# Optimization experiments

Measured on AMD Instinct MI355X. Metric: run time of the kernel, lower is better.

## Reference

```python
import jax, jax.numpy as jnp
import numpy as np

# S5 layer: ZOH discretization of diagonal complex SSM + parallel associative scan
# u: (B, L, H) real; state dim P (complex diagonal Lambda)

DT_MIN, DT_MAX = 1e-3, 1e-1
STEP_RESCALE = 1.0

def setup_inputs() -> dict:
    key = jax.random.key(0)
    ks = jax.random.split(key, 7)
    Bsz, L, H, P = 8, 4096, 1024, 512
    u = jax.random.normal(ks[0], (Bsz, L, H), jnp.float32)
    # HiPPO-like diagonal: negative real part, spread imaginary part
    Lambda_re = -0.5 * jnp.abs(jax.random.normal(ks[1], (P,), jnp.float32)) - 0.1
    Lambda_im = jnp.pi * jax.random.normal(ks[2], (P,), jnp.float32)
    # B: (P, H, 2) real/imag stacked (xavier-ish scale); C: (H, P, 2)
    Bp = jax.random.normal(ks[3], (P, H, 2), jnp.float32) / np.sqrt(H)
    Cp = jax.random.normal(ks[4], (H, P, 2), jnp.float32) / np.sqrt(P)
    D = jax.random.normal(ks[5], (H,), jnp.float32)
    log_step = jnp.log(jax.random.uniform(ks[6], (P, 1), jnp.float32) * (DT_MAX - DT_MIN) + DT_MIN)
    return {"u": u, "Lambda_re": Lambda_re, "Lambda_im": Lambda_im,
            "B": Bp, "C": Cp, "D": D, "log_step": log_step}


def _s5_forward(u, Lambda_re, Lambda_im, B, C, D, log_step):
    # clip_eigs=True: keep real part strictly negative
    Lambda = jnp.minimum(Lambda_re, -1e-4) + 1j * Lambda_im          # (P,)
    B_tilde = (B[..., 0] + 1j * B[..., 1]).astype(jnp.complex64)      # (P, H)
    C_tilde = (C[..., 0] + 1j * C[..., 1]).astype(jnp.complex64)      # (H, P)
    step = STEP_RESCALE * jnp.exp(log_step[:, 0])                     # (P,)
    # ZOH discretization
    Lambda_bar = jnp.exp(Lambda * step)                               # (P,)
    B_bar = ((Lambda_bar - 1.0) / Lambda)[:, None] * B_tilde          # (P, H)
    # input projection into state space
    Bu = jnp.einsum('blh,ph->blp', u.astype(jnp.complex64), B_bar)    # (B, L, P)
    A = jnp.broadcast_to(Lambda_bar, Bu.shape)                        # (B, L, P)
    # linear recurrence x_k = Lambda_bar * x_{k-1} + Bu_k via log-depth scan
    def combine(e_i, e_j):
        a_i, b_i = e_i
        a_j, b_j = e_j
        return a_j * a_i, a_j * b_i + b_j
    _, xs = jax.lax.associative_scan(combine, (A, Bu), axis=1)        # (B, L, P)
    # readout
    ys = jnp.einsum('blp,hp->blh', xs, C_tilde).real + D * u          # (B, L, H)
    return ys


def reference(u, Lambda_re, Lambda_im, B, C, D, log_step):
    return _s5_forward(u, Lambda_re, Lambda_im, B, C, D, log_step)
```

## Files before the change

kernel.cpp:

```cpp
#include <hip/hip_runtime.h>


#define Bsz 8
#define Lseq 4096
#define Hdim 1024
#define Pdim 512
#define NCHUNK 64
#define CHUNK 64
#define MROWS 32768

typedef __attribute__((ext_vector_type(8))) __bf16 bf16x8;
typedef __attribute__((ext_vector_type(4))) float f32x4;

__device__ __forceinline__ unsigned short f2bf(float f) {
  union { float f; unsigned u; } v; v.f = f;
  unsigned r = v.u + 0x7fffu + ((v.u >> 16) & 1u);
  return (unsigned short)(r >> 16);
}
__device__ __forceinline__ float bf2f(unsigned short s) {
  union { unsigned u; float f; } v; v.u = ((unsigned)s) << 16;
  return v.f;
}

__device__ __forceinline__ void gld_lds16(const void* g, void* l) {
  __builtin_amdgcn_global_load_lds(
      (const __attribute__((address_space(1))) unsigned int*)g,
      (__attribute__((address_space(3))) unsigned int*)l, 16, 0, 0);
}

__global__ void k_setup(const float* __restrict__ Lre_in, const float* __restrict__ Lim_in,
                        const float* __restrict__ log_step,
                        float2* __restrict__ a_arr, float2* __restrict__ aS_arr,
                        float2* __restrict__ g_arr) {
  int p = threadIdx.x;
  if (p >= Pdim) return;
  float lre = fminf(Lre_in[p], -1e-4f);
  float lim = Lim_in[p];
  float step = expf(log_step[p]);
  float zr = lre * step, zi = lim * step;
  float er = expf(zr);
  float ar = er * cosf(zi), ai = er * sinf(zi);
  a_arr[p] = make_float2(ar, ai);
  float erS = expf(zr * (float)CHUNK);
  aS_arr[p] = make_float2(erS * cosf(zi * (float)CHUNK), erS * sinf(zi * (float)CHUNK));
  float den = lre * lre + lim * lim;
  float nr = ar - 1.0f, ni = ai;
  g_arr[p] = make_float2((nr * lre + ni * lim) / den, (ni * lre - nr * lim) / den);
}

__global__ void k_prep_B(const float* __restrict__ Bin, const float2* __restrict__ g_arr,
                         unsigned short* __restrict__ Bbar2) {
  int idx = blockIdx.x * 256 + threadIdx.x;
  int p = idx >> 10;
  int h = idx & 1023;
  float B0 = Bin[2 * idx];
  float B1 = Bin[2 * idx + 1];
  float2 g = g_arr[p];
  Bbar2[(size_t)p * Hdim + h]            = f2bf(g.x * B0 - g.y * B1);
  Bbar2[(size_t)(Pdim + p) * Hdim + h]   = f2bf(g.x * B1 + g.y * B0);
}

__global__ void k_prep_C(const float* __restrict__ Cin, unsigned short* __restrict__ C2m) {
  int idx = blockIdx.x * 256 + threadIdx.x;
  int h = idx >> 9;
  int p = idx & 511;
  float C0 = Cin[2 * idx];
  float C1 = Cin[2 * idx + 1];
  C2m[(size_t)h * 1024 + p]        = f2bf(C0);
  C2m[(size_t)h * 1024 + 512 + p]  = f2bf(-C1);
}

__global__ void k_cvt_u(const float* __restrict__ u, unsigned short* __restrict__ ub) {
  size_t tidg = (size_t)blockIdx.x * 256 + threadIdx.x;
#pragma unroll 4
  for (int it = 0; it < 16; ++it) {
    size_t i = (tidg + (size_t)it * 524288) * 4;
    float4 v = *(const float4*)(u + i);
    ushort4 o;
    o.x = f2bf(v.x); o.y = f2bf(v.y); o.z = f2bf(v.z); o.w = f2bf(v.w);
    *(ushort4*)(ub + i) = o;
  }
}


#define STAGE_A(t_, bo_)                                                    \
  do {                                                                      \
    _Pragma("unroll")                                                       \
    for (int jj = 0; jj < 4; jj++)                                          \
      gld_lds16(pa[jj] + (t_) * 64, smc + (bo_) + (jj * 512 + tid) * 16);   \
  } while (0)

#define STAGE_B(t_, bo_)                                                    \
  do {                                                                      \
    _Pragma("unroll")                                                       \
    for (int jj = 0; jj < 4; jj++)                                          \
      gld_lds16(pb[jj] + (t_) * 64, smc + (bo_) + 32768 + (jj * 512 + tid) * 16); \
  } while (0)

#define PHASE_Q(mh, nh, LA, LB, PRE, POST)                                  \
  {                                                                         \
    const char* bb_ = smc + bufo;                                           \
    if (LA) {                                                               \
      _Pragma("unroll")                                                     \
      for (int i_ = 0; i_ < 4; i_++) {                                      \
        int rb_ = aRowByte + ((mh) * 4 + i_) * 2048;                        \
        af[i_][0] = *(const bf16x8*)(bb_ + rb_ + k0);                       \
        af[i_][1] = *(const bf16x8*)(bb_ + rb_ + k1);                       \
      }                                                                     \
    }                                                                       \
    if (LB) {                                                               \
      _Pragma("unroll")                                                     \
      for (int j_ = 0; j_ < 2; j_++) {                                      \
        int rb_ = bRowByte + ((nh) * 2 + j_) * 2048;                        \
        bfv[j_][0] = *(const bf16x8*)(bb_ + rb_ + k0);                      \
        bfv[j_][1] = *(const bf16x8*)(bb_ + rb_ + k1);                      \
      }                                                                     \
    }                                                                       \
    PRE;                                                                    \
    __builtin_amdgcn_s_barrier();                                           \
    asm volatile("s_waitcnt lgkmcnt(0)" ::: "memory");                      \
    __builtin_amdgcn_sched_barrier(0);                                      \
    __builtin_amdgcn_s_setprio(1);                                          \
    _Pragma("unroll")                                                       \
    for (int i_ = 0; i_ < 4; i_++)                                          \
      _Pragma("unroll")                                                     \
      for (int j_ = 0; j_ < 2; j_++) {                                      \
        acc[(mh) * 4 + i_][(nh) * 2 + j_] =                                 \
            __builtin_amdgcn_mfma_f32_16x16x32_bf16(                        \
                af[i_][0], bfv[j_][0], acc[(mh) * 4 + i_][(nh) * 2 + j_], 0, 0, 0); \
        acc[(mh) * 4 + i_][(nh) * 2 + j_] =                                 \
            __builtin_amdgcn_mfma_f32_16x16x32_bf16(                        \
                af[i_][1], bfv[j_][1], acc[(mh) * 4 + i_][(nh) * 2 + j_], 0, 0, 0); \
      }                                                                     \
    __builtin_amdgcn_s_setprio(0);                                          \
    POST;                                                                   \
    __builtin_amdgcn_s_barrier();                                           \
  }

template <int EPI>
__global__ __launch_bounds__(512, 2) void gemm256(const unsigned short* __restrict__ A,
                                                  const unsigned short* __restrict__ Bt,
                                                  void* __restrict__ Cout,
                                                  const float* __restrict__ uin,
                                                  const float* __restrict__ Dvec) {
  const int K = 1024;
  __shared__ __align__(16) unsigned short sm[65536];
  char* smc = (char*)sm;

  int tid = threadIdx.x;
  int lane = tid & 63;
  int w = tid >> 6;
  int wr = w >> 2, wc = w & 3;
  int quad = lane >> 4;
  int mrow = lane & 15;

  int wg = blockIdx.x;
  size_t rowBase = (size_t)(wg >> 2) * 256;
  size_t colBase = (size_t)(wg & 3) * 256;

  f32x4 acc[8][4];
#pragma unroll
  for (int i = 0; i < 8; i++)
#pragma unroll
    for (int j = 0; j < 4; j++) acc[i][j] = (f32x4){0.f, 0.f, 0.f, 0.f};

  bf16x8 af[4][2], bfv[2][2];

  int cs = (tid & 7) ^ ((tid >> 3) & 7);
  int rT = tid >> 3;
  const unsigned short* pa[4];
  const unsigned short* pb[4];
#pragma unroll
  for (int jj = 0; jj < 4; jj++) {
    pa[jj] = A  + (rowBase + jj * 64 + rT) * K + cs * 8;
    pb[jj] = Bt + (colBase + jj * 64 + rT) * K + cs * 8;
  }

  int axor = (mrow & 7) << 4;
  int k0 = (quad * 16) ^ axor;
  int k1 = (64 + quad * 16) ^ axor;
  int aRowByte = (wr * 128 + mrow) * 128;
  int bRowByte = 32768 + (wc * 64 + mrow) * 128;

  STAGE_A(0, 0);
  STAGE_B(0, 0);
  asm volatile("s_waitcnt vmcnt(0)" ::: "memory");
  __builtin_amdgcn_s_barrier();

  for (int t = 0; t < 16; ++t) {
    int bufo = (t & 1) * 65536;
    int nbo = bufo ^ 65536;
    PHASE_Q(0, 0, 1, 1, if (t < 15) STAGE_A(t + 1, nbo), );
    PHASE_Q(0, 1, 0, 1, if (t < 15) STAGE_B(t + 1, nbo), );
    PHASE_Q(1, 1, 1, 0, , );
    PHASE_Q(1, 0, 0, 1, , asm volatile("s_waitcnt vmcnt(0)" ::: "memory"));
  }

  if (EPI == 0) {
    unsigned short* O = (unsigned short*)Cout;
    __syncthreads();
#pragma unroll
    for (int fm = 0; fm < 8; fm++)
#pragma unroll
      for (int fn = 0; fn < 4; fn++)
#pragma unroll
        for (int r = 0; r < 4; r++) {
          int m_l = wr * 128 + fm * 16 + quad * 4 + r;
          int n_l = wc * 64 + fn * 16 + mrow;
          sm[m_l * 256 + n_l] = f2bf(acc[fm][fn][r]);
        }
    __syncthreads();
#pragma unroll
    for (int it = 0; it < 16; it++) {
      int cid = it * 512 + tid;
      int r = cid >> 5;
      int c = cid & 31;
      uint4 v = *(const uint4*)(sm + r * 256 + c * 8);
      *(uint4*)(O + (rowBase + r) * 1024 + colBase + c * 8) = v;
    }
  } else {
    float* O = (float*)Cout;
    size_t mBase = rowBase + wr * 128 + quad * 4;
    size_t nBase = colBase + wc * 64 + mrow;
#pragma unroll
    for (int fm = 0; fm < 8; fm++)
#pragma unroll
      for (int fn = 0; fn < 4; fn++) {
        size_t n = nBase + fn * 16;
        float dv = Dvec[n];
#pragma unroll
        for (int r = 0; r < 4; r++) {
          size_t m = mBase + fm * 16 + r;
          O[m * 1024 + n] = acc[fm][fn][r] + dv * uin[m * 1024 + n];
        }
      }
  }
}

__global__ void k_scan1(const unsigned short* __restrict__ Bu, const float2* __restrict__ a_arr,
                        float* __restrict__ carryT) {
  int bc = blockIdx.x;
  int p0 = threadIdx.x * 2;
  int b = bc >> 6, c = bc & 63;
  float2 a0 = a_arr[p0], a1 = a_arr[p0 + 1];
  const unsigned short* bu = Bu + ((size_t)b * Lseq + (size_t)c * CHUNK) * 1024;
  float tr0 = 0.f, ti0 = 0.f, tr1 = 0.f, ti1 = 0.f;
#pragma unroll 8
  for (int l = 0; l < CHUNK; l++) {
    unsigned vr = *(const unsigned*)(bu + (size_t)l * 1024 + p0);
    unsigned vi = *(const unsigned*)(bu + (size_t)l * 1024 + 512 + p0);
    float br0 = bf2f((unsigned short)vr), br1 = bf2f((unsigned short)(vr >> 16));
    float bi0 = bf2f((unsigned short)vi), bi1 = bf2f((unsigned short)(vi >> 16));
    float nr0 = fmaf(a0.x, tr0, fmaf(-a0.y, ti0, br0));
    ti0 = fmaf(a0.x, ti0, fmaf(a0.y, tr0, bi0));
    tr0 = nr0;
    float nr1 = fmaf(a1.x, tr1, fmaf(-a1.y, ti1, br1));
    ti1 = fmaf(a1.x, ti1, fmaf(a1.y, tr1, bi1));
    tr1 = nr1;
  }
  *(float2*)(carryT + (size_t)bc * 1024 + p0) = make_float2(tr0, tr1);
  *(float2*)(carryT + (size_t)bc * 1024 + 512 + p0) = make_float2(ti0, ti1);
}

__global__ void k_scan2(const float* __restrict__ carryT, const float2* __restrict__ aS_arr,
                        float* __restrict__ prefix) {
  int wid = blockIdx.x * 4 + (threadIdx.x >> 6);
  int lane = threadIdx.x & 63;
  int b = wid >> 9;
  int p = wid & 511;
  float2 s = aS_arr[p];
  size_t o = ((size_t)(b * NCHUNK + lane)) * 1024 + p;
  float tr = carryT[o], ti = carryT[o + 512];
  float mr = s.x, mi = s.y;
#pragma unroll
  for (int d = 1; d < 64; d <<= 1) {
    float ur = __shfl_up(tr, d, 64);
    float ui = __shfl_up(ti, d, 64);
    if (lane >= d) {
      tr = fmaf(mr, ur, fmaf(-mi, ui, tr));
      ti = fmaf(mr, ui, fmaf(mi, ur, ti));
    }
    float nmr = mr * mr - mi * mi;
    mi = 2.f * mr * mi;
    mr = nmr;
  }
  float er = __shfl_up(tr, 1, 64);
  float ei = __shfl_up(ti, 1, 64);
  if (lane == 0) { er = 0.f; ei = 0.f; }
  prefix[o] = er;
  prefix[o + 512] = ei;
}

__global__ void k_scan3(const unsigned short* __restrict__ Bu, const float2* __restrict__ a_arr,
                        const float* __restrict__ prefix, unsigned short* __restrict__ xs) {
  int bc = blockIdx.x;
  int p0 = threadIdx.x * 2;
  int b = bc >> 6, c = bc & 63;
  float2 a0 = a_arr[p0], a1 = a_arr[p0 + 1];
  size_t base = ((size_t)b * Lseq + (size_t)c * CHUNK) * 1024;
  size_t po = (size_t)bc * 1024 + p0;
  float2 xrv = *(const float2*)(prefix + po);
  float2 xiv = *(const float2*)(prefix + po + 512);
  float xr0 = xrv.x, xr1 = xrv.y, xi0 = xiv.x, xi1 = xiv.y;
#pragma unroll 8
  for (int l = 0; l < CHUNK; l++) {
    unsigned vr = *(const unsigned*)(Bu + base + (size_t)l * 1024 + p0);
    unsigned vi = *(const unsigned*)(Bu + base + (size_t)l * 1024 + 512 + p0);
    float br0 = bf2f((unsigned short)vr), br1 = bf2f((unsigned short)(vr >> 16));
    float bi0 = bf2f((unsigned short)vi), bi1 = bf2f((unsigned short)(vi >> 16));
    float nr0 = fmaf(a0.x, xr0, fmaf(-a0.y, xi0, br0));
    xi0 = fmaf(a0.x, xi0, fmaf(a0.y, xr0, bi0));
    xr0 = nr0;
    float nr1 = fmaf(a1.x, xr1, fmaf(-a1.y, xi1, br1));
    xi1 = fmaf(a1.x, xi1, fmaf(a1.y, xr1, bi1));
    xr1 = nr1;
    unsigned orv = (unsigned)f2bf(xr0) | ((unsigned)f2bf(xr1) << 16);
    unsigned oiv = (unsigned)f2bf(xi0) | ((unsigned)f2bf(xi1) << 16);
    *(unsigned*)(xs + base + (size_t)l * 1024 + p0) = orv;
    *(unsigned*)(xs + base + (size_t)l * 1024 + 512 + p0) = oiv;
  }
}

extern "C" void kernel_launch(void* const* d_in, const int* in_sizes, int n_in,
                              void* d_out, int out_size, void* d_ws, size_t ws_size,
                              hipStream_t stream) {
  const float* u     = (const float*)d_in[0];
  const float* Lre   = (const float*)d_in[1];
  const float* Lim   = (const float*)d_in[2];
  const float* Bin   = (const float*)d_in[3];
  const float* Cin   = (const float*)d_in[4];
  const float* Dvec  = (const float*)d_in[5];
  const float* lstep = (const float*)d_in[6];

  char* ws = (char*)d_ws;
  unsigned short* ubf_xs = (unsigned short*)(ws);
  unsigned short* Bbar2  = (unsigned short*)(ws + 67108864);
  unsigned short* C2m    = (unsigned short*)(ws + 69206016);
  float*          carryT = (float*)(ws + 71303168);
  float*          prefix = (float*)(ws + 73400320);
  float2*         a_arr  = (float2*)(ws + 75497472);
  float2*         aS_arr = (float2*)(ws + 75501568);
  float2*         g_arr  = (float2*)(ws + 75505664);

  unsigned short* Bu = (unsigned short*)d_out;

  k_setup<<<1, 512, 0, stream>>>(Lre, Lim, lstep, a_arr, aS_arr, g_arr);
  k_prep_B<<<2048, 256, 0, stream>>>(Bin, g_arr, Bbar2);
  k_prep_C<<<2048, 256, 0, stream>>>(Cin, C2m);
  k_cvt_u<<<2048, 256, 0, stream>>>(u, ubf_xs);

  gemm256<0><<<512, 512, 0, stream>>>(ubf_xs, Bbar2, (void*)Bu, nullptr, nullptr);

  k_scan1<<<512, 256, 0, stream>>>(Bu, a_arr, carryT);
  k_scan2<<<1024, 256, 0, stream>>>(carryT, aS_arr, prefix);
  k_scan3<<<512, 256, 0, stream>>>(Bu, a_arr, prefix, ubf_xs);

  gemm256<1><<<512, 512, 0, stream>>>(ubf_xs, C2m, d_out, u, Dvec);
}
```

Measured before the change: 461.6 us.

## Fuse chunk-carry scan into first GEMM epilogue with interleaved complex layout

Changes the Bbar and C matrix layouts so that real and imaginary parts of each state are interleaved in adjacent columns. The first GEMM can then compute each 64-row chunk's local recurrence carry directly from its output tile in shared memory, which removes the separate k_scan1 pass that re-read all of Bu from global memory. k_scan2 and k_scan3 now use packed float2 carries and interleaved bf16 pairs. The conversion kernel also becomes one float4 per thread with more blocks. The GEMM epilogue gets longer and serial, with 4 chunks × 128 states per block.

```diff
diff --git a/kernel.cpp b/kernel.cpp
--- a/kernel.cpp
+++ b/kernel.cpp
@@ -56,8 +56,8 @@
   float B0 = Bin[2 * idx];
   float B1 = Bin[2 * idx + 1];
   float2 g = g_arr[p];
-  Bbar2[(size_t)p * Hdim + h]            = f2bf(g.x * B0 - g.y * B1);
-  Bbar2[(size_t)(Pdim + p) * Hdim + h]   = f2bf(g.x * B1 + g.y * B0);
+  Bbar2[(size_t)(2 * p) * Hdim + h]     = f2bf(g.x * B0 - g.y * B1);
+  Bbar2[(size_t)(2 * p + 1) * Hdim + h] = f2bf(g.x * B1 + g.y * B0);
 }
 
 __global__ void k_prep_C(const float* __restrict__ Cin, unsigned short* __restrict__ C2m) {
@@ -66,20 +66,16 @@
   int p = idx & 511;
   float C0 = Cin[2 * idx];
   float C1 = Cin[2 * idx + 1];
-  C2m[(size_t)h * 1024 + p]        = f2bf(C0);
-  C2m[(size_t)h * 1024 + 512 + p]  = f2bf(-C1);
+  C2m[(size_t)h * 1024 + 2 * p]     = f2bf(C0);
+  C2m[(size_t)h * 1024 + 2 * p + 1] = f2bf(-C1);
 }
 
 __global__ void k_cvt_u(const float* __restrict__ u, unsigned short* __restrict__ ub) {
-  size_t tidg = (size_t)blockIdx.x * 256 + threadIdx.x;
-#pragma unroll 4
-  for (int it = 0; it < 16; ++it) {
-    size_t i = (tidg + (size_t)it * 524288) * 4;
-    float4 v = *(const float4*)(u + i);
-    ushort4 o;
-    o.x = f2bf(v.x); o.y = f2bf(v.y); o.z = f2bf(v.z); o.w = f2bf(v.w);
-    *(ushort4*)(ub + i) = o;
-  }
+  size_t i = ((size_t)blockIdx.x * 256 + threadIdx.x) * 4;
+  float4 v = *(const float4*)(u + i);
+  ushort4 o;
+  o.x = f2bf(v.x); o.y = f2bf(v.y); o.z = f2bf(v.z); o.w = f2bf(v.w);
+  *(ushort4*)(ub + i) = o;
 }
 
 
@@ -142,7 +138,9 @@
                                                   const unsigned short* __restrict__ Bt,
                                                   void* __restrict__ Cout,
                                                   const float* __restrict__ uin,
-                                                  const float* __restrict__ Dvec) {
+                                                  const float* __restrict__ Dvec,
+                                                  const float2* __restrict__ a_arr,
+                                                  float2* __restrict__ carry2) {
   const int K = 1024;
   __shared__ __align__(16) unsigned short sm[65536];
   char* smc = (char*)sm;
@@ -218,6 +216,25 @@
       uint4 v = *(const uint4*)(sm + r * 256 + c * 8);
       *(uint4*)(O + (rowBase + r) * 1024 + colBase + c * 8) = v;
     }
+    {
+      int ql = tid & 127;
+      int cc = tid >> 7;
+      int qg = (wg & 3) * 128 + ql;
+      float2 a = a_arr[qg];
+      const unsigned short* row = sm + (cc * 64) * 256 + 2 * ql;
+      float tr = 0.f, ti = 0.f;
+#pragma unroll 8
+      for (int l = 0; l < 64; l++) {
+        unsigned v = *(const unsigned*)(row + l * 256);
+        float br = bf2f((unsigned short)v), bi = bf2f((unsigned short)(v >> 16));
+        float nr = fmaf(a.x, tr, fmaf(-a.y, ti, br));
+        ti = fmaf(a.x, ti, fmaf(a.y, tr, bi));
+        tr = nr;
+      }
+      int b = (int)(rowBase >> 12);
+      int cg = (int)((rowBase & 4095) >> 6) + cc;
+      carry2[(size_t)(b * NCHUNK + cg) * 512 + qg] = make_float2(tr, ti);
+    }
   } else {
     float* O = (float*)Cout;
     size_t mBase = rowBase + wr * 128 + quad * 4;
@@ -237,40 +254,16 @@
   }
 }
 
-__global__ void k_scan1(const unsigned short* __restrict__ Bu, const float2* __restrict__ a_arr,
-                        float* __restrict__ carryT) {
-  int bc = blockIdx.x;
-  int p0 = threadIdx.x * 2;
-  int b = bc >> 6, c = bc & 63;
-  float2 a0 = a_arr[p0], a1 = a_arr[p0 + 1];
-  const unsigned short* bu = Bu + ((size_t)b * Lseq + (size_t)c * CHUNK) * 1024;
-  float tr0 = 0.f, ti0 = 0.f, tr1 = 0.f, ti1 = 0.f;
-#pragma unroll 8
-  for (int l = 0; l < CHUNK; l++) {
-    unsigned vr = *(const unsigned*)(bu + (size_t)l * 1024 + p0);
-    unsigned vi = *(const unsigned*)(bu + (size_t)l * 1024 + 512 + p0);
-    float br0 = bf2f((unsigned short)vr), br1 = bf2f((unsigned short)(vr >> 16));
-    float bi0 = bf2f((unsigned short)vi), bi1 = bf2f((unsigned short)(vi >> 16));
-    float nr0 = fmaf(a0.x, tr0, fmaf(-a0.y, ti0, br0));
-    ti0 = fmaf(a0.x, ti0, fmaf(a0.y, tr0, bi0));
-    tr0 = nr0;
-    float nr1 = fmaf(a1.x, tr1, fmaf(-a1.y, ti1, br1));
-    ti1 = fmaf(a1.x, ti1, fmaf(a1.y, tr1, bi1));
-    tr1 = nr1;
-  }
-  *(float2*)(carryT + (size_t)bc * 1024 + p0) = make_float2(tr0, tr1);
-  *(float2*)(carryT + (size_t)bc * 1024 + 512 + p0) = make_float2(ti0, ti1);
-}
-
-__global__ void k_scan2(const float* __restrict__ carryT, const float2* __restrict__ aS_arr,
-                        float* __restrict__ prefix) {
+__global__ void k_scan2(const float2* __restrict__ carry2, const float2* __restrict__ aS_arr,
+                        float2* __restrict__ prefix2) {
   int wid = blockIdx.x * 4 + (threadIdx.x >> 6);
   int lane = threadIdx.x & 63;
   int b = wid >> 9;
-  int p = wid & 511;
-  float2 s = aS_arr[p];
-  size_t o = ((size_t)(b * NCHUNK + lane)) * 1024 + p;
-  float tr = carryT[o], ti = carryT[o + 512];
+  int q = wid & 511;
+  float2 s = aS_arr[q];
+  size_t o = (size_t)(b * NCHUNK + lane) * 512 + q;
+  float2 T = carry2[o];
+  float tr = T.x, ti = T.y;
   float mr = s.x, mi = s.y;
 #pragma unroll
   for (int d = 1; d < 64; d <<= 1) {
@@ -287,37 +280,37 @@
   float er = __shfl_up(tr, 1, 64);
   float ei = __shfl_up(ti, 1, 64);
   if (lane == 0) { er = 0.f; ei = 0.f; }
-  prefix[o] = er;
-  prefix[o + 512] = ei;
+  prefix2[o] = make_float2(er, ei);
 }
 
 __global__ void k_scan3(const unsigned short* __restrict__ Bu, const float2* __restrict__ a_arr,
-                        const float* __restrict__ prefix, unsigned short* __restrict__ xs) {
+                        const float2* __restrict__ prefix2, unsigned short* __restrict__ xs) {
   int bc = blockIdx.x;
-  int p0 = threadIdx.x * 2;
+  int t = threadIdx.x;
+  int q0 = t, q1 = t + 256;
   int b = bc >> 6, c = bc & 63;
-  float2 a0 = a_arr[p0], a1 = a_arr[p0 + 1];
+  float2 a0 = a_arr[q0], a1 = a_arr[q1];
   size_t base = ((size_t)b * Lseq + (size_t)c * CHUNK) * 1024;
-  size_t po = (size_t)bc * 1024 + p0;
-  float2 xrv = *(const float2*)(prefix + po);
-  float2 xiv = *(const float2*)(prefix + po + 512);
-  float xr0 = xrv.x, xr1 = xrv.y, xi0 = xiv.x, xi1 = xiv.y;
+  size_t po = (size_t)bc * 512;
+  float2 x0 = prefix2[po + q0];
+  float2 x1 = prefix2[po + q1];
+  float xr0 = x0.x, xi0 = x0.y, xr1 = x1.x, xi1 = x1.y;
 #pragma unroll 8
   for (int l = 0; l < CHUNK; l++) {
-    unsigned vr = *(const unsigned*)(Bu + base + (size_t)l * 1024 + p0);
-    unsigned vi = *(const unsigned*)(Bu + base + (size_t)l * 1024 + 512 + p0);
-    float br0 = bf2f((unsigned short)vr), br1 = bf2f((unsigned short)(vr >> 16));
-    float bi0 = bf2f((unsigned short)vi), bi1 = bf2f((unsigned short)(vi >> 16));
+    unsigned v0 = *(const unsigned*)(Bu + base + (size_t)l * 1024 + 2 * q0);
+    unsigned v1 = *(const unsigned*)(Bu + base + (size_t)l * 1024 + 2 * q1);
+    float br0 = bf2f((unsigned short)v0), bi0 = bf2f((unsigned short)(v0 >> 16));
+    float br1 = bf2f((unsigned short)v1), bi1 = bf2f((unsigned short)(v1 >> 16));
     float nr0 = fmaf(a0.x, xr0, fmaf(-a0.y, xi0, br0));
     xi0 = fmaf(a0.x, xi0, fmaf(a0.y, xr0, bi0));
     xr0 = nr0;
     float nr1 = fmaf(a1.x, xr1, fmaf(-a1.y, xi1, br1));
     xi1 = fmaf(a1.x, xi1, fmaf(a1.y, xr1, bi1));
     xr1 = nr1;
-    unsigned orv = (unsigned)f2bf(xr0) | ((unsigned)f2bf(xr1) << 16);
-    unsigned oiv = (unsigned)f2bf(xi0) | ((unsigned)f2bf(xi1) << 16);
-    *(unsigned*)(xs + base + (size_t)l * 1024 + p0) = orv;
-    *(unsigned*)(xs + base + (size_t)l * 1024 + 512 + p0) = oiv;
+    unsigned o0 = (unsigned)f2bf(xr0) | ((unsigned)f2bf(xi0) << 16);
+    unsigned o1 = (unsigned)f2bf(xr1) | ((unsigned)f2bf(xi1) << 16);
+    *(unsigned*)(xs + base + (size_t)l * 1024 + 2 * q0) = o0;
+    *(unsigned*)(xs + base + (size_t)l * 1024 + 2 * q1) = o1;
   }
 }
 
@@ -336,8 +329,8 @@
   unsigned short* ubf_xs = (unsigned short*)(ws);
   unsigned short* Bbar2  = (unsigned short*)(ws + 67108864);
   unsigned short* C2m    = (unsigned short*)(ws + 69206016);
-  float*          carryT = (float*)(ws + 71303168);
-  float*          prefix = (float*)(ws + 73400320);
+  float2*         carry2 = (float2*)(ws + 71303168);
+  float2*         prefix2= (float2*)(ws + 73400320);
   float2*         a_arr  = (float2*)(ws + 75497472);
   float2*         aS_arr = (float2*)(ws + 75501568);
   float2*         g_arr  = (float2*)(ws + 75505664);
@@ -347,13 +340,13 @@
   k_setup<<<1, 512, 0, stream>>>(Lre, Lim, lstep, a_arr, aS_arr, g_arr);
   k_prep_B<<<2048, 256, 0, stream>>>(Bin, g_arr, Bbar2);
   k_prep_C<<<2048, 256, 0, stream>>>(Cin, C2m);
-  k_cvt_u<<<2048, 256, 0, stream>>>(u, ubf_xs);
-
-  gemm256<0><<<512, 512, 0, stream>>>(ubf_xs, Bbar2, (void*)Bu, nullptr, nullptr);
-
-  k_scan1<<<512, 256, 0, stream>>>(Bu, a_arr, carryT);
-  k_scan2<<<1024, 256, 0, stream>>>(carryT, aS_arr, prefix);
-  k_scan3<<<512, 256, 0, stream>>>(Bu, a_arr, prefix, ubf_xs);
-
-  gemm256<1><<<512, 512, 0, stream>>>(ubf_xs, C2m, d_out, u, Dvec);
-}
+  k_cvt_u<<<32768, 256, 0, stream>>>(u, ubf_xs);
+
+  gemm256<0><<<512, 512, 0, stream>>>(ubf_xs, Bbar2, (void*)Bu, nullptr, nullptr,
+                                      a_arr, carry2);
+
+  k_scan2<<<1024, 256, 0, stream>>>(carry2, aS_arr, prefix2);
+  k_scan3<<<512, 256, 0, stream>>>(Bu, a_arr, prefix2, ubf_xs);
+
+  gemm256<1><<<512, 512, 0, stream>>>(ubf_xs, C2m, d_out, u, Dvec, nullptr, nullptr);
+}
```

Measured after the change: 434.7 us. 1.06x faster.
